# Optimization experiments

Measured on AMD Instinct MI355X. Metric: run time of the kernel, lower is better.

## Reference

```python
import jax, jax.numpy as jnp
import numpy as np

B, A, E, H = 512, 4, 10, 256
OBS, PHY, G, MV = 2, 3, 3, 2
T = 10
STEP = 0.05


def setup_inputs() -> dict:
    key = jax.random.key(0)
    ks = jax.random.split(key, 16)
    rn = lambda k, s, sc=1.0: jax.random.normal(k, s, jnp.float32) * sc
    W = 0.1  # weight scale so tanh/sigmoid stay in sane range
    return {
        'observations': rn(ks[0], (B, A, E, OBS)),
        'physical': rn(ks[1], (B, E, PHY)),
        'observed_goals': rn(ks[2], (B, A, G)),
        'mem_physical': jnp.zeros((B, A, E, H), jnp.float32),
        'mem_action': jnp.zeros((B, A, H), jnp.float32),
        'W_ih_p': rn(ks[3], (3 * H, OBS + PHY), W),
        'W_hh_p': rn(ks[4], (3 * H, H), W),
        'b_ih_p': jnp.zeros((3 * H,), jnp.float32),
        'b_hh_p': jnp.zeros((3 * H,), jnp.float32),
        'W_fc_p': rn(ks[5], (H, H), W),
        'b_fc_p': jnp.zeros((H,), jnp.float32),
        'W_ih_a': rn(ks[6], (3 * H, H + G), W),
        'W_hh_a': rn(ks[7], (3 * H, H), W),
        'b_ih_a': jnp.zeros((3 * H,), jnp.float32),
        'b_hh_a': jnp.zeros((3 * H,), jnp.float32),
        'W_fc_a': rn(ks[8], (H, H), W),
        'b_fc_a': jnp.zeros((H,), jnp.float32),
        'W_m1': rn(ks[9], (H, H), W),
        'b_m1': jnp.zeros((H,), jnp.float32),
        'W_m2': rn(ks[10], (MV, H), W),
        'b_m2': jnp.zeros((MV,), jnp.float32),
    }


def _gru(x, h, Wih, Whh, bih, bhh):
    # torch.nn.GRUCell math, vectorized over leading dims
    gi = x @ Wih.T + bih
    gh = h @ Whh.T + bhh
    ir, iz, inn = jnp.split(gi, 3, axis=-1)
    hr, hz, hn = jnp.split(gh, 3, axis=-1)
    r = jax.nn.sigmoid(ir + hr)
    z = jax.nn.sigmoid(iz + hz)
    n = jnp.tanh(inn + r * hn)
    return (1.0 - z) * n + z * h


def reference(observations, physical, observed_goals, mem_physical, mem_action,
              W_ih_p, W_hh_p, b_ih_p, b_hh_p, W_fc_p, b_fc_p,
              W_ih_a, W_hh_a, b_ih_a, b_hh_a, W_fc_a, b_fc_a,
              W_m1, b_m1, W_m2, b_m2):
    b, a, e, _ = observations.shape
    # per-(agent, entity) input: cat(observation, entity physical features)
    phys_b = jnp.broadcast_to(physical[:, None], (b, a, e, physical.shape[-1]))
    x_p = jnp.concatenate([observations, phys_b], axis=-1)  # [B,A,E,5]

    def step(carry, _):
        mp, ma = carry  # [B,A,E,H], [B,A,H]
        # physical ProcessingModule over all (agent, entity) pairs at once
        h_p = _gru(x_p, mp, W_ih_p, W_hh_p, b_ih_p, b_hh_p)          # new 'physical' memory
        proc = jax.nn.elu(h_p @ W_fc_p.T + b_fc_p)                    # [B,A,E,H]
        feat = jnp.max(proc, axis=2)                                  # AdaptiveMaxPool2d((1,H)) over entities
        # ActionModule: GRU over cat(pooled physical feat, observed goal)
        x_a = jnp.concatenate([feat, observed_goals], axis=-1)       # [B,A,H+G]
        h_a = _gru(x_a, ma, W_ih_a, W_hh_a, b_ih_a, b_hh_a)          # new 'action' memory
        proc_a = jax.nn.elu(h_a @ W_fc_a.T + b_fc_a)
        mv = jnp.tanh(jax.nn.elu(proc_a @ W_m1.T + b_m1) @ W_m2.T + b_m2) * STEP  # [B,A,MV]
        return (h_p, h_a), mv

    _, movements = jax.lax.scan(step, (mem_physical, mem_action), None, length=T)
    return movements  # [T,B,A,MV]
```

## Files before the change

### kernel.cpp

```cpp
#include <hip/hip_runtime.h>
#include <math.h>

#define H 256
#define G3 768
#define BB 512
#define AA 4
#define EE 10
#define RP (BB*AA*EE)
#define RA (BB*AA)
#define TT 10
#define NMV 2
#define STEPSC 0.05f
#define DST 260
#define A1B 128
#define A2B 256
#define A3B 128
#define COMB 1280

typedef __attribute__((ext_vector_type(8))) short short8;
typedef __attribute__((ext_vector_type(8))) _Float16 half8;
typedef __attribute__((ext_vector_type(4))) float f32x4;

#if defined(__has_builtin)
#  if __has_builtin(__builtin_amdgcn_global_load_lds)
#    define HAS_GLL 1
#  endif
#endif

__device__ __forceinline__ float sigmoid_(float x){ return 1.f/(1.f + __expf(-x)); }
__device__ __forceinline__ float tanh_(float x){
    float ax = fabsf(x);
    float e  = __expf(-2.f*ax);
    float t  = (1.f - e)/(1.f + e);
    return copysignf(t, x);
}
__device__ __forceinline__ float elu_(float x){ return x > 0.f ? x : (__expf(x) - 1.f); }

#define MFMA16(A,B,C) __builtin_amdgcn_mfma_f32_16x16x32_f16(A,B,C,0,0,0)

__device__ __forceinline__ void cp16(const void* g, void* l) {
#ifdef HAS_GLL
    __builtin_amdgcn_global_load_lds(
        (const __attribute__((address_space(1))) unsigned int*)g,
        (__attribute__((address_space(3))) unsigned int*)l, 16, 0, 0);
#else
    *(short8*)l = *(const short8*)g;
#endif
}

__global__ void k_splitw(const float* __restrict__ src, _Float16* __restrict__ dst,
                         int n, int ldsrc)
{
    int i = blockIdx.x*256 + threadIdx.x;
    if (i < n) {
        int j  = i & 7;
        int l  = (i >> 3) & 63;
        int kc = (i >> 9) & 7;
        int c  = i >> 12;
        int row = c*16 + (l & 15);
        int k   = kc*32 + (l >> 4)*8 + j;
        dst[i] = (_Float16)src[(size_t)row*ldsrc + k];
    }
}

__global__ void k_gia_goal(const float* __restrict__ goals,
                           const float* __restrict__ Wiha,
                           const float* __restrict__ biha,
                           _Float16* __restrict__ out)
{
    int idx = blockIdx.x*256 + threadIdx.x;
    int ra = idx / G3, k = idx % G3;
    float g0 = goals[ra*3+0], g1 = goals[ra*3+1], g2 = goals[ra*3+2];
    const float* w = Wiha + (size_t)k*259 + 256;
    out[idx] = (_Float16)(biha[k] + g0*w[0] + g1*w[1] + g2*w[2]);
}

__global__ void k_cvt(const float* __restrict__ src, _Float16* __restrict__ dst, int n)
{
    int i = blockIdx.x*256 + threadIdx.x;
    if (i < n) dst[i] = (_Float16)src[i];
}

__global__ __launch_bounds__(256, 2)
void k_step(int gru_t, int fc_t, int a1_t, int a2_t, int a3_t,
            _Float16* __restrict__ hp0, _Float16* __restrict__ hp1,
            _Float16* __restrict__ proc0, _Float16* __restrict__ proc1,
            _Float16* __restrict__ ha0, _Float16* __restrict__ ha1,
            _Float16* __restrict__ pca0, _Float16* __restrict__ pca1,
            const _Float16* __restrict__ wWhh, const _Float16* __restrict__ wWfc,
            const _Float16* __restrict__ wWhha, const _Float16* __restrict__ wWiha,
            const _Float16* __restrict__ wWfca, const _Float16* __restrict__ wWm1,
            const _Float16* __restrict__ gia,
            const float* __restrict__ obs, const float* __restrict__ phys,
            const float* __restrict__ Wih, const float* __restrict__ bih,
            const float* __restrict__ bhh, const float* __restrict__ bfcp,
            const float* __restrict__ bhha, const float* __restrict__ bfca,
            const float* __restrict__ bm1,
            const float* __restrict__ Wm2, const float* __restrict__ bm2,
            float* __restrict__ out)
{
    __shared__ char smem[24576];
    int b = blockIdx.x;
    const int tid = threadIdx.x;
    const int wv = tid >> 6, lane = tid & 63;
    const int quad = lane >> 4, l16 = lane & 15;

    if (b < A1B) {
        if (a1_t < 0) return;
        float* D = (float*)smem;
        const _Float16* proc = (a1_t & 1) ? proc1 : proc0;
        const _Float16* hain = (a1_t & 1) ? ha1 : ha0;
        _Float16*      haout = (a1_t & 1) ? ha0 : ha1;
        const int ra0 = b*16;

        for (int i = tid; i < 16*32; i += 256) {
            int r = i >> 5, cg = (i & 31)*8;
            const _Float16* p = proc + ((size_t)(ra0 + r)*EE)*H + cg;
            half8 v = *(const half8*)p;
            float m[8];
            #pragma unroll
            for (int j = 0; j < 8; j++) m[j] = (float)v[j];
            #pragma unroll
            for (int e = 1; e < EE; e++) {
                half8 u = *(const half8*)(p + (size_t)e*H);
                #pragma unroll
                for (int j = 0; j < 8; j++) m[j] = fmaxf(m[j], (float)u[j]);
            }
            #pragma unroll
            for (int j = 0; j < 8; j++) D[r*DST + cg + j] = m[j];
        }
        __syncthreads();

        half8 Fh[8], Hh[8];
        #pragma unroll
        for (int kc = 0; kc < 8; kc++) {
            const float* fp = &D[l16*DST + quad*8 + kc*32];
            #pragma unroll
            for (int j = 0; j < 8; j++) Fh[kc][j] = (_Float16)fp[j];
            Hh[kc] = *(const half8*)(hain + (size_t)(ra0 + l16)*H + quad*8 + kc*32);
        }

        #pragma unroll
        for (int p = 0; p < 2; p++) {
            f32x4 gh[3][2], gx[3][2];
            #pragma unroll
            for (int g = 0; g < 3; g++)
                #pragma unroll
                for (int ch = 0; ch < 2; ch++) {
                    gh[g][ch] = (f32x4){0.f,0.f,0.f,0.f};
                    gx[g][ch] = (f32x4){0.f,0.f,0.f,0.f};
                }
            #pragma unroll
            for (int kc = 0; kc < 8; kc++)
                #pragma unroll
                for (int ch = 0; ch < 2; ch++)
                    #pragma unroll
                    for (int g = 0; g < 3; g++) {
                        const size_t cg = (size_t)(g*16 + wv*4 + p*2 + ch);
                        half8 bh = *(const half8*)(wWhha + (cg*8+kc)*512 + lane*8);
                        half8 bx = *(const half8*)(wWiha + (cg*8+kc)*512 + lane*8);
                        gh[g][ch] = MFMA16(Hh[kc], bh, gh[g][ch]);
                        gx[g][ch] = MFMA16(Fh[kc], bx, gx[g][ch]);
                    }
            #pragma unroll
            for (int ch = 0; ch < 2; ch++) {
                const int c = wv*64 + (p*2+ch)*16 + l16;
                const float br = bhha[c], bz = bhha[256+c], bn = bhha[512+c];
                #pragma unroll
                for (int reg = 0; reg < 4; reg++) {
                    const int r = quad*4 + reg;
                    const _Float16* gp = gia + (size_t)(ra0 + r)*G3;
                    float rg = sigmoid_((float)gp[c]     + gx[0][ch][reg] + gh[0][ch][reg] + br);
                    float z  = sigmoid_((float)gp[256+c] + gx[1][ch][reg] + gh[1][ch][reg] + bz);
                    float n  = tanh_((float)gp[512+c] + gx[2][ch][reg] + rg*(gh[2][ch][reg] + bn));
                    size_t idx = (size_t)(ra0 + r)*H + c;
                    float hprev = (float)hain[idx];
                    haout[idx] = (_Float16)((1.f - z)*n + z*hprev);
                }
            }
        }
        return;
    }
    b -= A1B;

    if (b < A2B) {
        if (a2_t < 0) return;
        const _Float16* hnew = (a2_t & 1) ? ha0 : ha1;
        _Float16*       pca  = (a2_t & 1) ? pca1 : pca0;
        const int ra0 = (b >> 1)*16;
        const int half = b & 1;

        half8 Hh[8];
        #pragma unroll
        for (int kc = 0; kc < 8; kc++)
            Hh[kc] = *(const half8*)(hnew + (size_t)(ra0 + l16)*H + quad*8 + kc*32);

        f32x4 ac[2];
        ac[0] = (f32x4){0.f,0.f,0.f,0.f};
        ac[1] = (f32x4){0.f,0.f,0.f,0.f};
        #pragma unroll
        for (int kc = 0; kc < 8; kc++)
            #pragma unroll
            for (int ch = 0; ch < 2; ch++) {
                const size_t cidx = (size_t)(half*8 + wv*2 + ch);
                half8 w = *(const half8*)(wWfca + (cidx*8+kc)*512 + lane*8);
                ac[ch] = MFMA16(Hh[kc], w, ac[ch]);
            }
        #pragma unroll
        for (int ch = 0; ch < 2; ch++) {
            const int c = (half*8 + wv*2 + ch)*16 + l16;
            const float bs = bfca[c];
            #pragma unroll
            for (int reg = 0; reg < 4; reg++) {
                int row = ra0 + quad*4 + reg;
                pca[(size_t)row*H + c] = (_Float16)elu_(ac[ch][reg] + bs);
            }
        }
        return;
    }
    b -= A2B;

    if (b < A3B) {
        if (a3_t < 0) return;
        float* D = (float*)smem;
        const _Float16* pca = (a3_t & 1) ? pca1 : pca0;
        const int ra0 = b*16;

        half8 Ph[8];
        #pragma unroll
        for (int kc = 0; kc < 8; kc++)
            Ph[kc] = *(const half8*)(pca + (size_t)(ra0 + l16)*H + quad*8 + kc*32);

        f32x4 ac[4];
        #pragma unroll
        for (int ch = 0; ch < 4; ch++) ac[ch] = (f32x4){0.f,0.f,0.f,0.f};
        #pragma unroll
        for (int kc = 0; kc < 8; kc++)
            #pragma unroll
            for (int ch = 0; ch < 4; ch++) {
                half8 w = *(const half8*)(wWm1 + ((size_t)(wv*4+ch)*8+kc)*512 + lane*8);
                ac[ch] = MFMA16(Ph[kc], w, ac[ch]);
            }
        #pragma unroll
        for (int ch = 0; ch < 4; ch++) {
            const int c = wv*64 + ch*16 + l16;
            const float bs = bm1[c];
            #pragma unroll
            for (int reg = 0; reg < 4; reg++)
                D[(quad*4+reg)*DST + c] = elu_(ac[ch][reg] + bs);
        }
        __syncthreads();

        if (tid < 32) {
            int r = tid >> 1, v = tid & 1;
            const float* w = Wm2 + (size_t)v*H;
            float s = bm2[v];
            #pragma unroll 4
            for (int i = 0; i < H/4; i++) {
                float4 a = *(const float4*)&D[r*DST + i*4];
                float4 c = *(const float4*)&w[i*4];
                s = fmaf(a.x,c.x,s); s = fmaf(a.y,c.y,s);
                s = fmaf(a.z,c.z,s); s = fmaf(a.w,c.w,s);
            }
            out[((size_t)a3_t*RA + ra0 + r)*NMV + v] = tanh_(s)*STEPSC;
        }
        return;
    }
    b -= A3B;

    {
        const bool do_gru = (gru_t >= 0);
        const bool do_fc  = (fc_t >= 0);
        if (!do_gru && !do_fc) return;
        _Float16* Bw = (_Float16*)smem;
        const int par = do_gru ? (gru_t & 1) : ((fc_t + 1) & 1);
        const _Float16* hin  = par ? hp1 : hp0;
        _Float16*       hout = par ? hp0 : hp1;
        _Float16*       pout = (fc_t & 1) ? proc1 : proc0;
        const int xm = b % 160, ys = b / 160;
        const int mt0 = xm*128 + wv*16;
        const int mt1 = mt0 + 64;

        half8 Ah[2][8];
        #pragma unroll
        for (int kc = 0; kc < 8; kc++) {
            Ah[0][kc] = *(const half8*)(hin + (size_t)(mt0 + l16)*H + quad*8 + kc*32);
            Ah[1][kc] = *(const half8*)(hin + (size_t)(mt1 + l16)*H + quad*8 + kc*32);
        }

        if (do_gru) {
            for (int s = 0; s < 2; s++) {
                const int cs = ys*2 + s;
                if (s) __syncthreads();
                #pragma unroll
                for (int k = 0; k < 6; k++) {
                    int i = tid + 256*k;
                    int g = i >> 9;
                    cp16(wWhh + (size_t)(g*16+cs)*4096 + (i & 511)*8, &Bw[(size_t)i*8]);
                }
                __syncthreads();

                f32x4 acc[2][3];
                #pragma unroll
                for (int mt = 0; mt < 2; mt++)
                    #pragma unroll
                    for (int g = 0; g < 3; g++) acc[mt][g] = (f32x4){0.f,0.f,0.f,0.f};
                #pragma unroll
                for (int kc = 0; kc < 8; kc++)
                    #pragma unroll
                    for (int g = 0; g < 3; g++) {
                        half8 w = *(const half8*)&Bw[(g*8 + kc)*512 + lane*8];
                        acc[0][g] = MFMA16(Ah[0][kc], w, acc[0][g]);
                        acc[1][g] = MFMA16(Ah[1][kc], w, acc[1][g]);
                    }

                const int col = cs*16 + l16;
                const float bhr = bhh[col], bhz = bhh[256+col], bhn = bhh[512+col];
                const float br_ = bih[col], bz_ = bih[256+col], bn_ = bih[512+col];
                const float* pr = Wih + (size_t)col*5;
                const float* pz = Wih + (size_t)(256+col)*5;
                const float* pn = Wih + (size_t)(512+col)*5;
                #pragma unroll
                for (int mt = 0; mt < 2; mt++) {
                    const int mb = mt ? mt1 : mt0;
                    #pragma unroll
                    for (int r = 0; r < 4; r++) {
                        int row = mb + quad*4 + r;
                        float2 ob = *(const float2*)(obs + (size_t)row*2);
                        int bb = row / (AA*EE), e = row % EE;
                        const float* pp = phys + (size_t)(bb*EE + e)*3;
                        float xv0 = ob.x, xv1 = ob.y, xv2 = pp[0], xv3 = pp[1], xv4 = pp[2];
                        float gr = br_, gz = bz_, gn = bn_;
                        gr = fmaf(xv0,pr[0],gr); gr = fmaf(xv1,pr[1],gr); gr = fmaf(xv2,pr[2],gr);
                        gr = fmaf(xv3,pr[3],gr); gr = fmaf(xv4,pr[4],gr);
                        gz = fmaf(xv0,pz[0],gz); gz = fmaf(xv1,pz[1],gz); gz = fmaf(xv2,pz[2],gz);
                        gz = fmaf(xv3,pz[3],gz); gz = fmaf(xv4,pz[4],gz);
                        gn = fmaf(xv0,pn[0],gn); gn = fmaf(xv1,pn[1],gn); gn = fmaf(xv2,pn[2],gn);
                        gn = fmaf(xv3,pn[3],gn); gn = fmaf(xv4,pn[4],gn);
                        float rg = sigmoid_(gr + acc[mt][0][r] + bhr);
                        float z  = sigmoid_(gz + acc[mt][1][r] + bhz);
                        float n  = tanh_(gn + rg*(acc[mt][2][r] + bhn));
                        size_t idx = (size_t)row*H + col;
                        float hprev = (float)hin[idx];
                        hout[idx] = (_Float16)((1.f - z)*n + z*hprev);
                    }
                }
            }
        }

        if (do_fc) {
            const int cs2 = ys;
            __syncthreads();
            #pragma unroll
            for (int k = 0; k < 4; k++) {
                int i = tid + 256*k;
                cp16(wWfc + (size_t)cs2*8192 + i*8, &Bw[(size_t)i*8]);
            }
            __syncthreads();

            f32x4 acc[2][2];
            #pragma unroll
            for (int mt = 0; mt < 2; mt++)
                #pragma unroll
                for (int ni = 0; ni < 2; ni++) acc[mt][ni] = (f32x4){0.f,0.f,0.f,0.f};
            #pragma unroll
            for (int kc = 0; kc < 8; kc++)
                #pragma unroll
                for (int ni = 0; ni < 2; ni++) {
                    half8 w = *(const half8*)&Bw[ni*4096 + kc*512 + lane*8];
                    acc[0][ni] = MFMA16(Ah[0][kc], w, acc[0][ni]);
                    acc[1][ni] = MFMA16(Ah[1][kc], w, acc[1][ni]);
                }
            #pragma unroll
            for (int mt = 0; mt < 2; mt++) {
                const int mb = mt ? mt1 : mt0;
                #pragma unroll
                for (int ni = 0; ni < 2; ni++) {
                    const int col = cs2*32 + ni*16 + l16;
                    const float bs = bfcp[col];
                    #pragma unroll
                    for (int r = 0; r < 4; r++) {
                        int row = mb + quad*4 + r;
                        pout[(size_t)row*H + col] = (_Float16)elu_(acc[mt][ni][r] + bs);
                    }
                }
            }
        }
    }
}

extern "C" void kernel_launch(void* const* d_in, const int* in_sizes, int n_in,
                              void* d_out, int out_size, void* d_ws, size_t ws_size,
                              hipStream_t stream)
{
    const float* obs  = (const float*)d_in[0];
    const float* phys = (const float*)d_in[1];
    const float* goals= (const float*)d_in[2];
    const float* memp = (const float*)d_in[3];
    const float* mema = (const float*)d_in[4];
    const float* Wihp = (const float*)d_in[5];
    const float* Whhp = (const float*)d_in[6];
    const float* bihp = (const float*)d_in[7];
    const float* bhhp = (const float*)d_in[8];
    const float* Wfcp = (const float*)d_in[9];
    const float* bfcp = (const float*)d_in[10];
    const float* Wiha = (const float*)d_in[11];
    const float* Whha = (const float*)d_in[12];
    const float* biha = (const float*)d_in[13];
    const float* bhha = (const float*)d_in[14];
    const float* Wfca = (const float*)d_in[15];
    const float* bfca = (const float*)d_in[16];
    const float* Wm1  = (const float*)d_in[17];
    const float* bm1  = (const float*)d_in[18];
    const float* Wm2  = (const float*)d_in[19];
    const float* bm2  = (const float*)d_in[20];
    float* out = (float*)d_out;
    (void)ws_size;

    char* base = (char*)d_ws;
    size_t off = 0;
    auto alloc = [&](size_t bytes) -> char* {
        char* p = base + off;
        off += (bytes + 255) & ~(size_t)255;
        return p;
    };
    _Float16* wp_whh = (_Float16*)alloc((size_t)G3*H*2);
    _Float16* wp_wfc = (_Float16*)alloc((size_t)H*H*2);
    _Float16* wa_whh = (_Float16*)alloc((size_t)G3*H*2);
    _Float16* wa_wih = (_Float16*)alloc((size_t)G3*H*2);
    _Float16* wa_wfc = (_Float16*)alloc((size_t)H*H*2);
    _Float16* wa_wm1 = (_Float16*)alloc((size_t)H*H*2);
    _Float16* gia    = (_Float16*)alloc((size_t)RA*G3*2);
    _Float16* hp0    = (_Float16*)alloc((size_t)RP*H*2);
    _Float16* hp1    = (_Float16*)alloc((size_t)RP*H*2);
    _Float16* proc0  = (_Float16*)alloc((size_t)RP*H*2);
    _Float16* proc1  = (_Float16*)alloc((size_t)RP*H*2);
    _Float16* ha0    = (_Float16*)alloc((size_t)RA*H*2);
    _Float16* ha1    = (_Float16*)alloc((size_t)RA*H*2);
    _Float16* pca0   = (_Float16*)alloc((size_t)RA*H*2);
    _Float16* pca1   = (_Float16*)alloc((size_t)RA*H*2);

    k_splitw<<<(G3*H+255)/256, 256, 0, stream>>>(Whhp, wp_whh, G3*H, H);
    k_splitw<<<(H*H+255)/256, 256, 0, stream>>>(Wfcp, wp_wfc, H*H, H);
    k_splitw<<<(G3*H+255)/256, 256, 0, stream>>>(Whha, wa_whh, G3*H, H);
    k_splitw<<<(G3*H+255)/256, 256, 0, stream>>>(Wiha, wa_wih, G3*H, 259);
    k_splitw<<<(H*H+255)/256, 256, 0, stream>>>(Wfca, wa_wfc, H*H, H);
    k_splitw<<<(H*H+255)/256, 256, 0, stream>>>(Wm1,  wa_wm1, H*H, H);
    k_gia_goal<<<RA*G3/256, 256, 0, stream>>>(goals, Wiha, biha, gia);
    k_cvt<<<((size_t)RP*H+255)/256, 256, 0, stream>>>(memp, hp0, RP*H);
    k_cvt<<<((size_t)RA*H+255)/256, 256, 0, stream>>>(mema, ha0, RA*H);

    const int NB = A1B + A2B + A3B + COMB;
    for (int L = 0; L <= TT + 3; L++) {
        int gru_t = (L <= TT-1) ? L : -1;
        int fc_t  = (L-1 >= 0 && L-1 <= TT-1) ? L-1 : -1;
        int a1_t  = (L-2 >= 0 && L-2 <= TT-1) ? L-2 : -1;
        int a2_t  = (L-3 >= 0 && L-3 <= TT-1) ? L-3 : -1;
        int a3_t  = (L-4 >= 0 && L-4 <= TT-1) ? L-4 : -1;
        k_step<<<NB, 256, 0, stream>>>(gru_t, fc_t, a1_t, a2_t, a3_t,
                                       hp0, hp1, proc0, proc1, ha0, ha1, pca0, pca1,
                                       wp_whh, wp_wfc, wa_whh, wa_wih, wa_wfc, wa_wm1,
                                       gia, obs, phys,
                                       Wihp, bihp, bhhp, bfcp,
                                       bhha, bfca, bm1, Wm2, bm2, out);
    }
}
```

Measured before the change: 644.0 us.

## Fuse action GRU, FC and MLP stages into one block to shorten pipeline

```diff
diff --git a/kernel.cpp b/kernel.cpp
--- a/kernel.cpp
+++ b/kernel.cpp
@@ -12,9 +12,7 @@
 #define NMV 2
 #define STEPSC 0.05f
 #define DST 260
-#define A1B 128
-#define A2B 256
-#define A3B 128
+#define FAB 128
 #define COMB 1280
 
 typedef __attribute__((ext_vector_type(8))) short short8;
@@ -82,11 +80,10 @@
 }
 
 __global__ __launch_bounds__(256, 2)
-void k_step(int gru_t, int fc_t, int a1_t, int a2_t, int a3_t,
+void k_step(int gru_t, int fc_t, int act_t,
             _Float16* __restrict__ hp0, _Float16* __restrict__ hp1,
             _Float16* __restrict__ proc0, _Float16* __restrict__ proc1,
             _Float16* __restrict__ ha0, _Float16* __restrict__ ha1,
-            _Float16* __restrict__ pca0, _Float16* __restrict__ pca1,
             const _Float16* __restrict__ wWhh, const _Float16* __restrict__ wWfc,
             const _Float16* __restrict__ wWhha, const _Float16* __restrict__ wWiha,
             const _Float16* __restrict__ wWfca, const _Float16* __restrict__ wWm1,
@@ -105,12 +102,12 @@
     const int wv = tid >> 6, lane = tid & 63;
     const int quad = lane >> 4, l16 = lane & 15;
 
-    if (b < A1B) {
-        if (a1_t < 0) return;
+    if (b < FAB) {
+        if (act_t < 0) return;
         float* D = (float*)smem;
-        const _Float16* proc = (a1_t & 1) ? proc1 : proc0;
-        const _Float16* hain = (a1_t & 1) ? ha1 : ha0;
-        _Float16*      haout = (a1_t & 1) ? ha0 : ha1;
+        const _Float16* proc = (act_t & 1) ? proc1 : proc0;
+        const _Float16* hain = (act_t & 1) ? ha1 : ha0;
+        _Float16*      haout = (act_t & 1) ? ha0 : ha1;
         const int ra0 = b*16;
 
         for (int i = tid; i < 16*32; i += 256) {
@@ -179,75 +176,60 @@
                 }
             }
         }
-        return;
-    }
-    b -= A1B;
-
-    if (b < A2B) {
-        if (a2_t < 0) return;
-        const _Float16* hnew = (a2_t & 1) ? ha0 : ha1;
-        _Float16*       pca  = (a2_t & 1) ? pca1 : pca0;
-        const int ra0 = (b >> 1)*16;
-        const int half = b & 1;
-
-        half8 Hh[8];
+        __threadfence_block();
+        __syncthreads();
+
         #pragma unroll
         for (int kc = 0; kc < 8; kc++)
-            Hh[kc] = *(const half8*)(hnew + (size_t)(ra0 + l16)*H + quad*8 + kc*32);
-
-        f32x4 ac[2];
-        ac[0] = (f32x4){0.f,0.f,0.f,0.f};
-        ac[1] = (f32x4){0.f,0.f,0.f,0.f};
+            Hh[kc] = *(const half8*)(haout + (size_t)(ra0 + l16)*H + quad*8 + kc*32);
+        {
+            f32x4 ac[4];
+            #pragma unroll
+            for (int ch = 0; ch < 4; ch++) ac[ch] = (f32x4){0.f,0.f,0.f,0.f};
+            #pragma unroll
+            for (int kc = 0; kc < 8; kc++)
+                #pragma unroll
+                for (int ch = 0; ch < 4; ch++) {
+                    half8 w = *(const half8*)(wWfca + ((size_t)(wv*4+ch)*8+kc)*512 + lane*8);
+                    ac[ch] = MFMA16(Hh[kc], w, ac[ch]);
+                }
+            #pragma unroll
+            for (int ch = 0; ch < 4; ch++) {
+                const int c = wv*64 + ch*16 + l16;
+                const float bs = bfca[c];
+                #pragma unroll
+                for (int reg = 0; reg < 4; reg++)
+                    D[(quad*4+reg)*DST + c] = elu_(ac[ch][reg] + bs);
+            }
+        }
+        __syncthreads();
+
         #pragma unroll
-        for (int kc = 0; kc < 8; kc++)
-            #pragma unroll
-            for (int ch = 0; ch < 2; ch++) {
-                const size_t cidx = (size_t)(half*8 + wv*2 + ch);
-                half8 w = *(const half8*)(wWfca + (cidx*8+kc)*512 + lane*8);
-                ac[ch] = MFMA16(Hh[kc], w, ac[ch]);
-            }
-        #pragma unroll
-        for (int ch = 0; ch < 2; ch++) {
-            const int c = (half*8 + wv*2 + ch)*16 + l16;
-            const float bs = bfca[c];
-            #pragma unroll
-            for (int reg = 0; reg < 4; reg++) {
-                int row = ra0 + quad*4 + reg;
-                pca[(size_t)row*H + c] = (_Float16)elu_(ac[ch][reg] + bs);
-            }
-        }
-        return;
-    }
-    b -= A2B;
-
-    if (b < A3B) {
-        if (a3_t < 0) return;
-        float* D = (float*)smem;
-        const _Float16* pca = (a3_t & 1) ? pca1 : pca0;
-        const int ra0 = b*16;
-
-        half8 Ph[8];
-        #pragma unroll
-        for (int kc = 0; kc < 8; kc++)
-            Ph[kc] = *(const half8*)(pca + (size_t)(ra0 + l16)*H + quad*8 + kc*32);
-
-        f32x4 ac[4];
-        #pragma unroll
-        for (int ch = 0; ch < 4; ch++) ac[ch] = (f32x4){0.f,0.f,0.f,0.f};
-        #pragma unroll
-        for (int kc = 0; kc < 8; kc++)
+        for (int kc = 0; kc < 8; kc++) {
+            const float* fp = &D[l16*DST + quad*8 + kc*32];
+            #pragma unroll
+            for (int j = 0; j < 8; j++) Fh[kc][j] = (_Float16)fp[j];
+        }
+        __syncthreads();
+        {
+            f32x4 ac[4];
+            #pragma unroll
+            for (int ch = 0; ch < 4; ch++) ac[ch] = (f32x4){0.f,0.f,0.f,0.f};
+            #pragma unroll
+            for (int kc = 0; kc < 8; kc++)
+                #pragma unroll
+                for (int ch = 0; ch < 4; ch++) {
+                    half8 w = *(const half8*)(wWm1 + ((size_t)(wv*4+ch)*8+kc)*512 + lane*8);
+                    ac[ch] = MFMA16(Fh[kc], w, ac[ch]);
+                }
             #pragma unroll
             for (int ch = 0; ch < 4; ch++) {
-                half8 w = *(const half8*)(wWm1 + ((size_t)(wv*4+ch)*8+kc)*512 + lane*8);
-                ac[ch] = MFMA16(Ph[kc], w, ac[ch]);
-            }
-        #pragma unroll
-        for (int ch = 0; ch < 4; ch++) {
-            const int c = wv*64 + ch*16 + l16;
-            const float bs = bm1[c];
-            #pragma unroll
-            for (int reg = 0; reg < 4; reg++)
-                D[(quad*4+reg)*DST + c] = elu_(ac[ch][reg] + bs);
+                const int c = wv*64 + ch*16 + l16;
+                const float bs = bm1[c];
+                #pragma unroll
+                for (int reg = 0; reg < 4; reg++)
+                    D[(quad*4+reg)*DST + c] = elu_(ac[ch][reg] + bs);
+            }
         }
         __syncthreads();
 
@@ -262,11 +244,11 @@
                 s = fmaf(a.x,c.x,s); s = fmaf(a.y,c.y,s);
                 s = fmaf(a.z,c.z,s); s = fmaf(a.w,c.w,s);
             }
-            out[((size_t)a3_t*RA + ra0 + r)*NMV + v] = tanh_(s)*STEPSC;
+            out[((size_t)act_t*RA + ra0 + r)*NMV + v] = tanh_(s)*STEPSC;
         }
         return;
     }
-    b -= A3B;
+    b -= FAB;
 
     {
         const bool do_gru = (gru_t >= 0);
@@ -437,8 +419,6 @@
     _Float16* proc1  = (_Float16*)alloc((size_t)RP*H*2);
     _Float16* ha0    = (_Float16*)alloc((size_t)RA*H*2);
     _Float16* ha1    = (_Float16*)alloc((size_t)RA*H*2);
-    _Float16* pca0   = (_Float16*)alloc((size_t)RA*H*2);
-    _Float16* pca1   = (_Float16*)alloc((size_t)RA*H*2);
 
     k_splitw<<<(G3*H+255)/256, 256, 0, stream>>>(Whhp, wp_whh, G3*H, H);
     k_splitw<<<(H*H+255)/256, 256, 0, stream>>>(Wfcp, wp_wfc, H*H, H);
@@ -450,15 +430,13 @@
     k_cvt<<<((size_t)RP*H+255)/256, 256, 0, stream>>>(memp, hp0, RP*H);
     k_cvt<<<((size_t)RA*H+255)/256, 256, 0, stream>>>(mema, ha0, RA*H);
 
-    const int NB = A1B + A2B + A3B + COMB;
-    for (int L = 0; L <= TT + 3; L++) {
+    const int NB = FAB + COMB;
+    for (int L = 0; L <= TT + 1; L++) {
         int gru_t = (L <= TT-1) ? L : -1;
         int fc_t  = (L-1 >= 0 && L-1 <= TT-1) ? L-1 : -1;
-        int a1_t  = (L-2 >= 0 && L-2 <= TT-1) ? L-2 : -1;
-        int a2_t  = (L-3 >= 0 && L-3 <= TT-1) ? L-3 : -1;
-        int a3_t  = (L-4 >= 0 && L-4 <= TT-1) ? L-4 : -1;
-        k_step<<<NB, 256, 0, stream>>>(gru_t, fc_t, a1_t, a2_t, a3_t,
-                                       hp0, hp1, proc0, proc1, ha0, ha1, pca0, pca1,
+        int act_t = (L-2 >= 0 && L-2 <= TT-1) ? L-2 : -1;
+        k_step<<<NB, 256, 0, stream>>>(gru_t, fc_t, act_t,
+                                       hp0, hp1, proc0, proc1, ha0, ha1,
                                        wp_whh, wp_wfc, wa_whh, wa_wih, wa_wfc, wa_wm1,
                                        gia, obs, phys,
                                        Wihp, bihp, bhhp, bfcp,
```

Result: slower. 786.8 us (+22.2%).
